# Kernel tuning notes

Measured on AMD Instinct MI355X. Metric: run time of the kernel, lower is better.

The kernel has to match this reference:

```python
import jax, jax.numpy as jnp
import numpy as np

N = 100000
E = 3200000
D_IN = 128
H = 32   # 2 * out_channels
OUT = 16 # out_channels


def _glorot(key, shape):
    lim = np.sqrt(6.0 / (shape[0] + shape[1]))
    return jax.random.uniform(key, shape, jnp.float32, -lim, lim)


def setup_inputs() -> dict:
    key = jax.random.key(0)
    ks = jax.random.split(key, 8)
    x = jax.random.normal(ks[0], (N, D_IN), jnp.float32)
    edge_index = jax.random.randint(ks[1], (2, E), 0, N, jnp.int64)
    W1 = _glorot(ks[2], (D_IN, H));  b1 = jnp.zeros((H,), jnp.float32)
    Wm = _glorot(ks[3], (H, OUT));   bm = jnp.zeros((OUT,), jnp.float32)
    Wv = _glorot(ks[4], (H, 1));     bv = jnp.zeros((1,), jnp.float32)
    return {"x": x, "edge_index": edge_index,
            "W1": W1, "b1": b1, "Wm": Wm, "bm": bm, "Wv": Wv, "bv": bv}


def _gcn_norm(edge_index, n_nodes):
    # add self-loops, then symmetric normalization D^-1/2 (A+I) D^-1/2
    loop = jnp.arange(n_nodes, dtype=edge_index.dtype)
    src = jnp.concatenate([edge_index[0], loop])
    dst = jnp.concatenate([edge_index[1], loop])
    deg = jax.ops.segment_sum(jnp.ones_like(dst, jnp.float32), dst,
                              num_segments=n_nodes)
    dinv = jnp.where(deg > 0, jax.lax.rsqrt(deg), 0.0)
    norm = dinv[src] * dinv[dst]  # [E + N]
    return src, dst, norm


def _gcn_conv(h, W, b, src, dst, norm, n_nodes):
    h = h @ W                                   # [N, out]
    msg = norm[:, None] * h[src]                # gather + scale, [E+N, out]
    out = jax.ops.segment_sum(msg, dst, num_segments=n_nodes)  # scatter-add
    return out + b


def reference(x, edge_index, W1, b1, Wm, bm, Wv, bv):
    src, dst, norm = _gcn_norm(edge_index, N)
    h = jax.nn.relu(_gcn_conv(x, W1, b1, src, dst, norm, N))
    mean = _gcn_conv(h, Wm, bm, src, dst, norm, N)
    mean = mean / jnp.linalg.norm(mean, axis=-1, keepdims=True)
    var = _gcn_conv(h, Wv, bv, src, dst, norm, N)
    var = jax.nn.softplus(var) + 1.0
    return mean, var
```

## Files before the change

### kernel.cpp

```cpp
#include <hip/hip_runtime.h>
#include <math.h>

#define N_NODES   100000
#define N_HALF    50000
#define N_EDGES   3200000
#define D_IN      128
#define H_DIM     32
#define OUT_DIM   16
#define NB        391
#define B1        1024
#define CHUNK     3125
#define NHIST     (NB * B1)
#define SUMS_N    (NHIST / 256)
#define SCANB_PER ((SUMS_N + 255) / 256)

typedef _Float16 half_t;
typedef __attribute__((ext_vector_type(4))) _Float16 half4;
typedef __attribute__((ext_vector_type(8))) _Float16 half8;


__global__ __launch_bounds__(256) void k_p1_hist(const int* __restrict__ dst,
                                                 int* __restrict__ hist_g) {
    __shared__ int hist[NB];
    int t = threadIdx.x;
    for (int i = t; i < NB; i += 256) hist[i] = 0;
    __syncthreads();
    int base = blockIdx.x * CHUNK;
    for (int k = t; k < CHUNK; k += 256)
        atomicAdd(&hist[dst[base + k] >> 8], 1);
    __syncthreads();
    for (int i = t; i < NB; i += 256) hist_g[i * B1 + blockIdx.x] = hist[i];
}


__global__ __launch_bounds__(256) void k_scanA(const int* __restrict__ hist_g,
                                               int* __restrict__ sums) {
    __shared__ int s[256];
    int t = threadIdx.x;
    s[t] = hist_g[blockIdx.x * 256 + t];
    __syncthreads();
    for (int off = 128; off > 0; off >>= 1) {
        if (t < off) s[t] += s[t + off];
        __syncthreads();
    }
    if (t == 0) sums[blockIdx.x] = s[0];
}

__global__ __launch_bounds__(256) void k_scanB(int* sums) {
    __shared__ int a[256], b[256];
    int t = threadIdx.x;
    int base = t * SCANB_PER;
    int v[SCANB_PER];
    int tot = 0;
#pragma unroll
    for (int k = 0; k < SCANB_PER; ++k) {
        v[k] = (base + k < SUMS_N) ? sums[base + k] : 0;
        tot += v[k];
    }
    a[t] = tot;
    __syncthreads();
    int* cur = a; int* nxt = b;
    for (int off = 1; off < 256; off <<= 1) {
        nxt[t] = cur[t] + ((t >= off) ? cur[t - off] : 0);
        __syncthreads();
        int* tmp = cur; cur = nxt; nxt = tmp;
    }
    int run = cur[t] - tot;
#pragma unroll
    for (int k = 0; k < SCANB_PER; ++k) {
        if (base + k < SUMS_N) sums[base + k] = run;
        run += v[k];
    }
}

__global__ __launch_bounds__(256) void k_scanC(int* hist_g, const int* __restrict__ sums) {
    __shared__ int a[256], b[256];
    int t = threadIdx.x;
    int v = hist_g[blockIdx.x * 256 + t];
    a[t] = v;
    __syncthreads();
    int* cur = a; int* nxt = b;
    for (int off = 1; off < 256; off <<= 1) {
        nxt[t] = cur[t] + ((t >= off) ? cur[t - off] : 0);
        __syncthreads();
        int* tmp = cur; cur = nxt; nxt = tmp;
    }
    hist_g[blockIdx.x * 256 + t] = sums[blockIdx.x] + cur[t] - v;
}


__global__ __launch_bounds__(256) void k_p3(const int* __restrict__ src,
                                            const int* __restrict__ dst,
                                            const int* __restrict__ hist_g,
                                            unsigned int* __restrict__ pairs) {
    __shared__ int cur[NB];
    int t = threadIdx.x;
    for (int i = t; i < NB; i += 256) cur[i] = hist_g[i * B1 + blockIdx.x];
    __syncthreads();
    int base = blockIdx.x * CHUNK;
    for (int k = t; k < CHUNK; k += 256) {
        int e = base + k;
        int d = dst[e];
        int pos = atomicAdd(&cur[d >> 8], 1);
        pairs[pos] = ((unsigned int)(d & 255) << 17) | (unsigned int)src[e];
    }
}


__global__ __launch_bounds__(512) void k_p4(const unsigned int* __restrict__ pairs,
                                            const int* __restrict__ hist_g,
                                            int* __restrict__ csr_src,
                                            int* __restrict__ row_ptr,
                                            int* __restrict__ row_mid,
                                            float* __restrict__ dinv) {
    __shared__ int cnt[512], a[512], b[512], cur[512];
    int t = threadIdx.x;
    int bk = blockIdx.x;
    int lo = hist_g[bk * B1];
    int hi = (bk + 1 < NB) ? hist_g[(bk + 1) * B1] : N_EDGES;

    cnt[t] = 0;
    __syncthreads();
    for (int j = lo + t; j < hi; j += 512) {
        unsigned int p = pairs[j];
        int s = (int)(p & 0x1FFFFu);
        int bin = (int)((p >> 17) << 1) | (s >= N_HALF);
        atomicAdd(&cnt[bin], 1);
    }
    __syncthreads();

    a[t] = cnt[t];
    __syncthreads();
    int* c0 = a; int* c1 = b;
    for (int off = 1; off < 512; off <<= 1) {
        c1[t] = c0[t] + ((t >= off) ? c0[t - off] : 0);
        __syncthreads();
        int* tmp = c0; c0 = c1; c1 = tmp;
    }
    int excl = c0[t] - cnt[t];
    cur[t] = lo + excl;

    int node = bk * 256 + (t >> 1);
    if (node < N_NODES) {
        if ((t & 1) == 0) {
            row_ptr[node] = lo + excl;
            dinv[node] = rsqrtf((float)(cnt[t] + cnt[t + 1]) + 1.0f);
        } else {
            row_mid[node] = lo + excl;
        }
    }
    if (bk == NB - 1 && t == 0) row_ptr[N_NODES] = N_EDGES;
    __syncthreads();

    for (int j = lo + t; j < hi; j += 512) {
        unsigned int p = pairs[j];
        int s = (int)(p & 0x1FFFFu);
        int bin = (int)((p >> 17) << 1) | (s >= N_HALF);
        int pos = atomicAdd(&cur[bin], 1);
        csr_src[pos] = s;
    }
}


__global__ __launch_bounds__(256) void k_gemm1(const float* __restrict__ x,
                                               const float* __restrict__ W1,
                                               const float* __restrict__ dinv,
                                               half_t* __restrict__ hs) {
    int i = blockIdx.x * 256 + threadIdx.x;
    if (i >= N_NODES) return;

    const float* xr = x + (size_t)i * D_IN;
    float acc[H_DIM];
#pragma unroll
    for (int c = 0; c < H_DIM; ++c) acc[c] = 0.f;

    for (int k0 = 0; k0 < D_IN; k0 += 4) {
        float4 xv = *(const float4*)(xr + k0);
#pragma unroll
        for (int kk = 0; kk < 4; ++kk) {
            float xk = (kk == 0) ? xv.x : (kk == 1) ? xv.y : (kk == 2) ? xv.z : xv.w;
            const float* wr = W1 + (k0 + kk) * H_DIM;
#pragma unroll
            for (int c = 0; c < H_DIM; ++c)
                acc[c] = fmaf(xk, wr[c], acc[c]);
        }
    }

    float di = dinv[i];
    half_t* o = hs + (size_t)i * H_DIM;
#pragma unroll
    for (int c4 = 0; c4 < H_DIM / 4; ++c4) {
        half4 ov;
        ov.x = (half_t)(acc[c4 * 4 + 0] * di);
        ov.y = (half_t)(acc[c4 * 4 + 1] * di);
        ov.z = (half_t)(acc[c4 * 4 + 2] * di);
        ov.w = (half_t)(acc[c4 * 4 + 3] * di);
        *(half4*)(o + c4 * 4) = ov;
    }
}


__global__ __launch_bounds__(256) void k_gather1A(const int* __restrict__ row_ptr,
                                                  const int* __restrict__ row_mid,
                                                  const int* __restrict__ csr_src,
                                                  const half_t* __restrict__ hs,
                                                  half_t* __restrict__ h_part) {
    int t = blockIdx.x * 256 + threadIdx.x;
    int i = t >> 2, c = t & 3;
    if (i >= N_NODES) return;

    const half8* hp = (const half8*)hs;
    int start = row_ptr[i], end = row_mid[i];
    float acc[8];
#pragma unroll
    for (int k = 0; k < 8; ++k) acc[k] = 0.f;

    int j = start;
    for (; j + 8 <= end; j += 8) {
        int s0 = csr_src[j + 0], s1 = csr_src[j + 1], s2 = csr_src[j + 2], s3 = csr_src[j + 3];
        int s4 = csr_src[j + 4], s5 = csr_src[j + 5], s6 = csr_src[j + 6], s7 = csr_src[j + 7];
        half8 v0 = hp[(size_t)s0 * 4 + c];
        half8 v1 = hp[(size_t)s1 * 4 + c];
        half8 v2 = hp[(size_t)s2 * 4 + c];
        half8 v3 = hp[(size_t)s3 * 4 + c];
        half8 v4 = hp[(size_t)s4 * 4 + c];
        half8 v5 = hp[(size_t)s5 * 4 + c];
        half8 v6 = hp[(size_t)s6 * 4 + c];
        half8 v7 = hp[(size_t)s7 * 4 + c];
#pragma unroll
        for (int k = 0; k < 8; ++k)
            acc[k] += ((float)v0[k] + (float)v1[k] + (float)v2[k] + (float)v3[k])
                    + ((float)v4[k] + (float)v5[k] + (float)v6[k] + (float)v7[k]);
    }
    for (; j < end; ++j) {
        int s = csr_src[j];
        half8 v = hp[(size_t)s * 4 + c];
#pragma unroll
        for (int k = 0; k < 8; ++k) acc[k] += (float)v[k];
    }

    half8 o;
#pragma unroll
    for (int k = 0; k < 8; ++k) o[k] = (half_t)acc[k];
    ((half8*)h_part)[(size_t)i * 4 + c] = o;
}


__global__ __launch_bounds__(256) void k_gather1B(const int* __restrict__ row_ptr,
                                                  const int* __restrict__ row_mid,
                                                  const int* __restrict__ csr_src,
                                                  const float* __restrict__ dinv,
                                                  const half_t* __restrict__ hs,
                                                  const half_t* __restrict__ h_part,
                                                  const float* __restrict__ b1,
                                                  half_t* __restrict__ h) {
    int t = blockIdx.x * 256 + threadIdx.x;
    int i = t >> 2, c = t & 3;
    if (i >= N_NODES) return;

    const half8* hp = (const half8*)hs;
    int start = row_mid[i], end = row_ptr[i + 1];
    half8 pv = ((const half8*)h_part)[(size_t)i * 4 + c];
    half8 sv = hp[(size_t)i * 4 + c];
    float acc[8];
#pragma unroll
    for (int k = 0; k < 8; ++k) acc[k] = (float)pv[k] + (float)sv[k];

    int j = start;
    for (; j + 8 <= end; j += 8) {
        int s0 = csr_src[j + 0], s1 = csr_src[j + 1], s2 = csr_src[j + 2], s3 = csr_src[j + 3];
        int s4 = csr_src[j + 4], s5 = csr_src[j + 5], s6 = csr_src[j + 6], s7 = csr_src[j + 7];
        half8 v0 = hp[(size_t)s0 * 4 + c];
        half8 v1 = hp[(size_t)s1 * 4 + c];
        half8 v2 = hp[(size_t)s2 * 4 + c];
        half8 v3 = hp[(size_t)s3 * 4 + c];
        half8 v4 = hp[(size_t)s4 * 4 + c];
        half8 v5 = hp[(size_t)s5 * 4 + c];
        half8 v6 = hp[(size_t)s6 * 4 + c];
        half8 v7 = hp[(size_t)s7 * 4 + c];
#pragma unroll
        for (int k = 0; k < 8; ++k)
            acc[k] += ((float)v0[k] + (float)v1[k] + (float)v2[k] + (float)v3[k])
                    + ((float)v4[k] + (float)v5[k] + (float)v6[k] + (float)v7[k]);
    }
    for (; j < end; ++j) {
        int s = csr_src[j];
        half8 v = hp[(size_t)s * 4 + c];
#pragma unroll
        for (int k = 0; k < 8; ++k) acc[k] += (float)v[k];
    }

    float di = dinv[i];
    float4 ba = *(const float4*)(b1 + c * 8);
    float4 bb = *(const float4*)(b1 + c * 8 + 4);
    half8 o;
    o[0] = (half_t)fmaxf(di * acc[0] + ba.x, 0.f);
    o[1] = (half_t)fmaxf(di * acc[1] + ba.y, 0.f);
    o[2] = (half_t)fmaxf(di * acc[2] + ba.z, 0.f);
    o[3] = (half_t)fmaxf(di * acc[3] + ba.w, 0.f);
    o[4] = (half_t)fmaxf(di * acc[4] + bb.x, 0.f);
    o[5] = (half_t)fmaxf(di * acc[5] + bb.y, 0.f);
    o[6] = (half_t)fmaxf(di * acc[6] + bb.z, 0.f);
    o[7] = (half_t)fmaxf(di * acc[7] + bb.w, 0.f);
    ((half8*)h)[(size_t)i * 4 + c] = o;
}


__global__ __launch_bounds__(256) void k_gemm2(const half_t* __restrict__ h,
                                               const float* __restrict__ Wm,
                                               const float* __restrict__ Wv,
                                               const float* __restrict__ dinv,
                                               half_t* __restrict__ hmv,
                                               float* __restrict__ varr) {
    int i = blockIdx.x * 256 + threadIdx.x;
    if (i >= N_NODES) return;

    const half4* hp = (const half4*)(h + (size_t)i * H_DIM);
    float acc[OUT_DIM + 1];
#pragma unroll
    for (int c = 0; c <= OUT_DIM; ++c) acc[c] = 0.f;

#pragma unroll
    for (int k4 = 0; k4 < H_DIM / 4; ++k4) {
        half4 v = hp[k4];
#pragma unroll
        for (int kk = 0; kk < 4; ++kk) {
            int k = k4 * 4 + kk;
            float hv = (kk == 0) ? (float)v.x : (kk == 1) ? (float)v.y
                     : (kk == 2) ? (float)v.z : (float)v.w;
            const float* wr = Wm + k * OUT_DIM;
#pragma unroll
            for (int c = 0; c < OUT_DIM; ++c)
                acc[c] = fmaf(hv, wr[c], acc[c]);
            acc[OUT_DIM] = fmaf(hv, Wv[k], acc[OUT_DIM]);
        }
    }

    float di = dinv[i];
    half_t* o = hmv + (size_t)i * OUT_DIM;
#pragma unroll
    for (int c4 = 0; c4 < OUT_DIM / 4; ++c4) {
        half4 ov;
        ov.x = (half_t)(acc[c4 * 4 + 0] * di);
        ov.y = (half_t)(acc[c4 * 4 + 1] * di);
        ov.z = (half_t)(acc[c4 * 4 + 2] * di);
        ov.w = (half_t)(acc[c4 * 4 + 3] * di);
        *(half4*)(o + c4 * 4) = ov;
    }
    varr[i] = acc[OUT_DIM] * di;
}


__global__ __launch_bounds__(256) void k_gather2f(const int* __restrict__ row_ptr,
                                                  const int* __restrict__ csr_src,
                                                  const float* __restrict__ dinv,
                                                  const half_t* __restrict__ hmv,
                                                  const float* __restrict__ varr,
                                                  const float* __restrict__ bm,
                                                  const float* __restrict__ bv,
                                                  float* __restrict__ out) {
    int t = blockIdx.x * 256 + threadIdx.x;
    int i = t >> 2, c = t & 3;
    if (i >= N_NODES) return;

    int start = row_ptr[i], end = row_ptr[i + 1];
    half4 sv = *(const half4*)(hmv + (size_t)i * OUT_DIM + c * 4);
    float a0 = (float)sv.x, a1 = (float)sv.y, a2 = (float)sv.z, a3 = (float)sv.w;
    float va = (c == 0) ? varr[i] : 0.f;

    int j = start;
    for (; j + 8 <= end; j += 8) {
        int s0 = csr_src[j + 0], s1 = csr_src[j + 1], s2 = csr_src[j + 2], s3 = csr_src[j + 3];
        int s4 = csr_src[j + 4], s5 = csr_src[j + 5], s6 = csr_src[j + 6], s7 = csr_src[j + 7];
        half4 v0 = *(const half4*)(hmv + (size_t)s0 * OUT_DIM + c * 4);
        half4 v1 = *(const half4*)(hmv + (size_t)s1 * OUT_DIM + c * 4);
        half4 v2 = *(const half4*)(hmv + (size_t)s2 * OUT_DIM + c * 4);
        half4 v3 = *(const half4*)(hmv + (size_t)s3 * OUT_DIM + c * 4);
        half4 v4 = *(const half4*)(hmv + (size_t)s4 * OUT_DIM + c * 4);
        half4 v5 = *(const half4*)(hmv + (size_t)s5 * OUT_DIM + c * 4);
        half4 v6 = *(const half4*)(hmv + (size_t)s6 * OUT_DIM + c * 4);
        half4 v7 = *(const half4*)(hmv + (size_t)s7 * OUT_DIM + c * 4);
        a0 += ((float)v0.x + (float)v1.x + (float)v2.x + (float)v3.x)
            + ((float)v4.x + (float)v5.x + (float)v6.x + (float)v7.x);
        a1 += ((float)v0.y + (float)v1.y + (float)v2.y + (float)v3.y)
            + ((float)v4.y + (float)v5.y + (float)v6.y + (float)v7.y);
        a2 += ((float)v0.z + (float)v1.z + (float)v2.z + (float)v3.z)
            + ((float)v4.z + (float)v5.z + (float)v6.z + (float)v7.z);
        a3 += ((float)v0.w + (float)v1.w + (float)v2.w + (float)v3.w)
            + ((float)v4.w + (float)v5.w + (float)v6.w + (float)v7.w);
        int sa = (c == 0) ? s0 : (c == 1) ? s1 : (c == 2) ? s2 : s3;
        int sb = (c == 0) ? s4 : (c == 1) ? s5 : (c == 2) ? s6 : s7;
        va += varr[sa] + varr[sb];
    }
    for (; j < end; ++j) {
        int s = csr_src[j];
        half4 v = *(const half4*)(hmv + (size_t)s * OUT_DIM + c * 4);
        a0 += (float)v.x; a1 += (float)v.y; a2 += (float)v.z; a3 += (float)v.w;
        if (c == 0) va += varr[s];
    }

    float di = dinv[i];
    float4 bb = *(const float4*)(bm + c * 4);
    float r0 = di * a0 + bb.x;
    float r1 = di * a1 + bb.y;
    float r2 = di * a2 + bb.z;
    float r3 = di * a3 + bb.w;
    float ssp = r0 * r0 + r1 * r1 + r2 * r2 + r3 * r3;
    ssp += __shfl_xor(ssp, 1, 4);
    ssp += __shfl_xor(ssp, 2, 4);
    va  += __shfl_xor(va, 1, 4);
    va  += __shfl_xor(va, 2, 4);
    float inv = rsqrtf(ssp);

    float4 o;
    o.x = r0 * inv; o.y = r1 * inv; o.z = r2 * inv; o.w = r3 * inv;
    *(float4*)(out + (size_t)i * OUT_DIM + c * 4) = o;
    if (c == 0) {
        float xv = di * va + bv[0];
        float sp = fmaxf(xv, 0.f) + log1pf(expf(-fabsf(xv)));
        out[(size_t)N_NODES * OUT_DIM + i] = sp + 1.0f;
    }
}


extern "C" void kernel_launch(void* const* d_in, const int* in_sizes, int n_in,
                              void* d_out, int out_size, void* d_ws, size_t ws_size,
                              hipStream_t stream) {
    const float* x  = (const float*)d_in[0];
    const int*   ei = (const int*)d_in[1];
    const float* W1 = (const float*)d_in[2];
    const float* b1 = (const float*)d_in[3];
    const float* Wm = (const float*)d_in[4];
    const float* bm = (const float*)d_in[5];
    const float* Wv = (const float*)d_in[6];
    const float* bv = (const float*)d_in[7];
    float* out = (float*)d_out;

    const int* src = ei;
    const int* dst = ei + N_EDGES;

    int*   wsi     = (int*)d_ws;
    int*   csr_src = wsi;
    int*   row_ptr = csr_src + N_EDGES;
    int*   row_mid = row_ptr + N_NODES + 1;
    float* dinv    = (float*)(row_mid + N_NODES);
    int*   hist_g  = (int*)(dinv + N_NODES);
    int*   sums    = hist_g + NHIST;
    size_t off     = (size_t)(sums + 2048 - wsi);
    off = (off + 3) & ~(size_t)3;
    unsigned int* pairs = (unsigned int*)(wsi + off);
    half_t* hs     = (half_t*)pairs;
    half_t* h      = hs + (size_t)N_NODES * H_DIM;
    half_t* hmv    = h + (size_t)N_NODES * H_DIM;
    float*  varr   = (float*)(hmv + (size_t)N_NODES * OUT_DIM);
    half_t* h_part = (half_t*)(varr + N_NODES);

    const int B = 256;
    int gN  = (N_NODES + B - 1) / B;
    int gN4 = (N_NODES * 4 + B - 1) / B;

    k_p1_hist<<<B1, B, 0, stream>>>(dst, hist_g);
    k_scanA<<<SUMS_N, B, 0, stream>>>(hist_g, sums);
    k_scanB<<<1, B, 0, stream>>>(sums);
    k_scanC<<<SUMS_N, B, 0, stream>>>(hist_g, sums);
    k_p3<<<B1, B, 0, stream>>>(src, dst, hist_g, pairs);
    k_p4<<<NB, 512, 0, stream>>>(pairs, hist_g, csr_src, row_ptr, row_mid, dinv);

    k_gemm1<<<gN, B, 0, stream>>>(x, W1, dinv, hs);
    k_gather1A<<<gN4, B, 0, stream>>>(row_ptr, row_mid, csr_src, hs, h_part);
    k_gather1B<<<gN4, B, 0, stream>>>(row_ptr, row_mid, csr_src, dinv, hs, h_part, b1, h);

    k_gemm2<<<gN, B, 0, stream>>>(h, Wm, Wv, dinv, hmv, varr);
    k_gather2f<<<gN4, B, 0, stream>>>(row_ptr, csr_src, dinv, hmv, varr, bm, bv, out);
}
```

Baseline: 311.1 us.

## Vectorize CSR build loads, halve sort blocks, widen gathers and gather2 lanes

Halves the number of histogram/scatter blocks (each now covers a larger chunk) and switches their edge reads to int4 vector loads with a scalar tail. The bucket-local sort in p4 is unrolled two-way. Layer-1 gathers now issue 16 independent row loads per step, and the final gather uses 2 lanes of 8 halves per node instead of 4 lanes of 4. The aim is fewer, wider memory transactions and more loads in flight, at the cost of lower block-level parallelism in the sort phases and higher register pressure.

```diff
diff --git a/kernel.cpp b/kernel.cpp
--- a/kernel.cpp
+++ b/kernel.cpp
@@ -8,15 +8,17 @@
 #define H_DIM     32
 #define OUT_DIM   16
 #define NB        391
-#define B1        1024
-#define CHUNK     3125
+#define B1        512
+#define CHUNK     6272
 #define NHIST     (NB * B1)
 #define SUMS_N    (NHIST / 256)
-#define SCANB_PER ((SUMS_N + 255) / 256)
+#define SCANB_PER 4
 
 typedef _Float16 half_t;
 typedef __attribute__((ext_vector_type(4))) _Float16 half4;
 typedef __attribute__((ext_vector_type(8))) _Float16 half8;
+
+#define PACK(d, s) ((((unsigned int)(d) & 255u) << 17) | (unsigned int)(s))
 
 
 __global__ __launch_bounds__(256) void k_p1_hist(const int* __restrict__ dst,
@@ -26,8 +28,19 @@
     for (int i = t; i < NB; i += 256) hist[i] = 0;
     __syncthreads();
     int base = blockIdx.x * CHUNK;
-    for (int k = t; k < CHUNK; k += 256)
-        atomicAdd(&hist[dst[base + k] >> 8], 1);
+    for (int k = t * 4; k < CHUNK; k += 1024) {
+        int e = base + k;
+        if (k + 4 <= CHUNK && e + 4 <= N_EDGES) {
+            int4 d = *(const int4*)(dst + e);
+            atomicAdd(&hist[d.x >> 8], 1);
+            atomicAdd(&hist[d.y >> 8], 1);
+            atomicAdd(&hist[d.z >> 8], 1);
+            atomicAdd(&hist[d.w >> 8], 1);
+        } else {
+            for (int kk = k; kk < CHUNK && base + kk < N_EDGES; ++kk)
+                atomicAdd(&hist[dst[base + kk] >> 8], 1);
+        }
+    }
     __syncthreads();
     for (int i = t; i < NB; i += 256) hist_g[i * B1 + blockIdx.x] = hist[i];
 }
@@ -98,11 +111,26 @@
     for (int i = t; i < NB; i += 256) cur[i] = hist_g[i * B1 + blockIdx.x];
     __syncthreads();
     int base = blockIdx.x * CHUNK;
-    for (int k = t; k < CHUNK; k += 256) {
+    for (int k = t * 4; k < CHUNK; k += 1024) {
         int e = base + k;
-        int d = dst[e];
-        int pos = atomicAdd(&cur[d >> 8], 1);
-        pairs[pos] = ((unsigned int)(d & 255) << 17) | (unsigned int)src[e];
+        if (k + 4 <= CHUNK && e + 4 <= N_EDGES) {
+            int4 d = *(const int4*)(dst + e);
+            int4 s = *(const int4*)(src + e);
+            int p0 = atomicAdd(&cur[d.x >> 8], 1);
+            int p1 = atomicAdd(&cur[d.y >> 8], 1);
+            int p2 = atomicAdd(&cur[d.z >> 8], 1);
+            int p3 = atomicAdd(&cur[d.w >> 8], 1);
+            pairs[p0] = PACK(d.x, s.x);
+            pairs[p1] = PACK(d.y, s.y);
+            pairs[p2] = PACK(d.z, s.z);
+            pairs[p3] = PACK(d.w, s.w);
+        } else {
+            for (int kk = k; kk < CHUNK && base + kk < N_EDGES; ++kk) {
+                int d = dst[base + kk];
+                int pos = atomicAdd(&cur[d >> 8], 1);
+                pairs[pos] = PACK(d, src[base + kk]);
+            }
+        }
     }
 }
 
@@ -121,11 +149,19 @@
 
     cnt[t] = 0;
     __syncthreads();
-    for (int j = lo + t; j < hi; j += 512) {
-        unsigned int p = pairs[j];
-        int s = (int)(p & 0x1FFFFu);
-        int bin = (int)((p >> 17) << 1) | (s >= N_HALF);
-        atomicAdd(&cnt[bin], 1);
+    {
+        int j = lo + t;
+        for (; j + 512 < hi; j += 1024) {
+            unsigned int p = pairs[j], q = pairs[j + 512];
+            int sp = (int)(p & 0x1FFFFu), sq = (int)(q & 0x1FFFFu);
+            atomicAdd(&cnt[(int)((p >> 17) << 1) | (sp >= N_HALF)], 1);
+            atomicAdd(&cnt[(int)((q >> 17) << 1) | (sq >= N_HALF)], 1);
+        }
+        for (; j < hi; j += 512) {
+            unsigned int p = pairs[j];
+            int sp = (int)(p & 0x1FFFFu);
+            atomicAdd(&cnt[(int)((p >> 17) << 1) | (sp >= N_HALF)], 1);
+        }
     }
     __syncthreads();
 
@@ -152,12 +188,22 @@
     if (bk == NB - 1 && t == 0) row_ptr[N_NODES] = N_EDGES;
     __syncthreads();
 
-    for (int j = lo + t; j < hi; j += 512) {
-        unsigned int p = pairs[j];
-        int s = (int)(p & 0x1FFFFu);
-        int bin = (int)((p >> 17) << 1) | (s >= N_HALF);
-        int pos = atomicAdd(&cur[bin], 1);
-        csr_src[pos] = s;
+    {
+        int j = lo + t;
+        for (; j + 512 < hi; j += 1024) {
+            unsigned int p = pairs[j], q = pairs[j + 512];
+            int sp = (int)(p & 0x1FFFFu), sq = (int)(q & 0x1FFFFu);
+            int pp = atomicAdd(&cur[(int)((p >> 17) << 1) | (sp >= N_HALF)], 1);
+            int pq = atomicAdd(&cur[(int)((q >> 17) << 1) | (sq >= N_HALF)], 1);
+            csr_src[pp] = sp;
+            csr_src[pq] = sq;
+        }
+        for (; j < hi; j += 512) {
+            unsigned int p = pairs[j];
+            int sp = (int)(p & 0x1FFFFu);
+            int pp = atomicAdd(&cur[(int)((p >> 17) << 1) | (sp >= N_HALF)], 1);
+            csr_src[pp] = sp;
+        }
     }
 }
 
@@ -197,6 +243,37 @@
         ov.w = (half_t)(acc[c4 * 4 + 3] * di);
         *(half4*)(o + c4 * 4) = ov;
     }
+}
+
+
+__device__ __forceinline__ void acc16(const half8* __restrict__ hp,
+                                      const int* __restrict__ csr, int j, int c,
+                                      float acc[8]) {
+    int s[16];
+#pragma unroll
+    for (int u = 0; u < 16; ++u) s[u] = csr[j + u];
+    half8 v[16];
+#pragma unroll
+    for (int u = 0; u < 16; ++u) v[u] = hp[(size_t)s[u] * 4 + c];
+#pragma unroll
+    for (int u = 0; u < 16; ++u)
+#pragma unroll
+        for (int k = 0; k < 8; ++k) acc[k] += (float)v[u][k];
+}
+
+__device__ __forceinline__ void acc4(const half8* __restrict__ hp,
+                                     const int* __restrict__ csr, int j, int c,
+                                     float acc[8]) {
+    int s[4];
+#pragma unroll
+    for (int u = 0; u < 4; ++u) s[u] = csr[j + u];
+    half8 v[4];
+#pragma unroll
+    for (int u = 0; u < 4; ++u) v[u] = hp[(size_t)s[u] * 4 + c];
+#pragma unroll
+    for (int u = 0; u < 4; ++u)
+#pragma unroll
+        for (int k = 0; k < 8; ++k) acc[k] += (float)v[u][k];
 }
 
 
@@ -216,25 +293,10 @@
     for (int k = 0; k < 8; ++k) acc[k] = 0.f;
 
     int j = start;
-    for (; j + 8 <= end; j += 8) {
-        int s0 = csr_src[j + 0], s1 = csr_src[j + 1], s2 = csr_src[j + 2], s3 = csr_src[j + 3];
-        int s4 = csr_src[j + 4], s5 = csr_src[j + 5], s6 = csr_src[j + 6], s7 = csr_src[j + 7];
-        half8 v0 = hp[(size_t)s0 * 4 + c];
-        half8 v1 = hp[(size_t)s1 * 4 + c];
-        half8 v2 = hp[(size_t)s2 * 4 + c];
-        half8 v3 = hp[(size_t)s3 * 4 + c];
-        half8 v4 = hp[(size_t)s4 * 4 + c];
-        half8 v5 = hp[(size_t)s5 * 4 + c];
-        half8 v6 = hp[(size_t)s6 * 4 + c];
-        half8 v7 = hp[(size_t)s7 * 4 + c];
-#pragma unroll
-        for (int k = 0; k < 8; ++k)
-            acc[k] += ((float)v0[k] + (float)v1[k] + (float)v2[k] + (float)v3[k])
-                    + ((float)v4[k] + (float)v5[k] + (float)v6[k] + (float)v7[k]);
-    }
+    for (; j + 16 <= end; j += 16) acc16(hp, csr_src, j, c, acc);
+    for (; j + 4 <= end; j += 4)  acc4(hp, csr_src, j, c, acc);
     for (; j < end; ++j) {
-        int s = csr_src[j];
-        half8 v = hp[(size_t)s * 4 + c];
+        half8 v = hp[(size_t)csr_src[j] * 4 + c];
 #pragma unroll
         for (int k = 0; k < 8; ++k) acc[k] += (float)v[k];
     }
@@ -267,25 +329,10 @@
     for (int k = 0; k < 8; ++k) acc[k] = (float)pv[k] + (float)sv[k];
 
     int j = start;
-    for (; j + 8 <= end; j += 8) {
-        int s0 = csr_src[j + 0], s1 = csr_src[j + 1], s2 = csr_src[j + 2], s3 = csr_src[j + 3];
-        int s4 = csr_src[j + 4], s5 = csr_src[j + 5], s6 = csr_src[j + 6], s7 = csr_src[j + 7];
-        half8 v0 = hp[(size_t)s0 * 4 + c];
-        half8 v1 = hp[(size_t)s1 * 4 + c];
-        half8 v2 = hp[(size_t)s2 * 4 + c];
-        half8 v3 = hp[(size_t)s3 * 4 + c];
-        half8 v4 = hp[(size_t)s4 * 4 + c];
-        half8 v5 = hp[(size_t)s5 * 4 + c];
-        half8 v6 = hp[(size_t)s6 * 4 + c];
-        half8 v7 = hp[(size_t)s7 * 4 + c];
-#pragma unroll
-        for (int k = 0; k < 8; ++k)
-            acc[k] += ((float)v0[k] + (float)v1[k] + (float)v2[k] + (float)v3[k])
-                    + ((float)v4[k] + (float)v5[k] + (float)v6[k] + (float)v7[k]);
-    }
+    for (; j + 16 <= end; j += 16) acc16(hp, csr_src, j, c, acc);
+    for (; j + 4 <= end; j += 4)  acc4(hp, csr_src, j, c, acc);
     for (; j < end; ++j) {
-        int s = csr_src[j];
-        half8 v = hp[(size_t)s * 4 + c];
+        half8 v = hp[(size_t)csr_src[j] * 4 + c];
 #pragma unroll
         for (int k = 0; k < 8; ++k) acc[k] += (float)v[k];
     }
@@ -360,61 +407,62 @@
                                                   const float* __restrict__ bv,
                                                   float* __restrict__ out) {
     int t = blockIdx.x * 256 + threadIdx.x;
-    int i = t >> 2, c = t & 3;
+    int i = t >> 1, c = t & 1;
     if (i >= N_NODES) return;
 
+    const half8* mp = (const half8*)hmv;
     int start = row_ptr[i], end = row_ptr[i + 1];
-    half4 sv = *(const half4*)(hmv + (size_t)i * OUT_DIM + c * 4);
-    float a0 = (float)sv.x, a1 = (float)sv.y, a2 = (float)sv.z, a3 = (float)sv.w;
+    half8 sv = mp[(size_t)i * 2 + c];
+    float acc[8];
+#pragma unroll
+    for (int k = 0; k < 8; ++k) acc[k] = (float)sv[k];
     float va = (c == 0) ? varr[i] : 0.f;
 
     int j = start;
     for (; j + 8 <= end; j += 8) {
-        int s0 = csr_src[j + 0], s1 = csr_src[j + 1], s2 = csr_src[j + 2], s3 = csr_src[j + 3];
-        int s4 = csr_src[j + 4], s5 = csr_src[j + 5], s6 = csr_src[j + 6], s7 = csr_src[j + 7];
-        half4 v0 = *(const half4*)(hmv + (size_t)s0 * OUT_DIM + c * 4);
-        half4 v1 = *(const half4*)(hmv + (size_t)s1 * OUT_DIM + c * 4);
-        half4 v2 = *(const half4*)(hmv + (size_t)s2 * OUT_DIM + c * 4);
-        half4 v3 = *(const half4*)(hmv + (size_t)s3 * OUT_DIM + c * 4);
-        half4 v4 = *(const half4*)(hmv + (size_t)s4 * OUT_DIM + c * 4);
-        half4 v5 = *(const half4*)(hmv + (size_t)s5 * OUT_DIM + c * 4);
-        half4 v6 = *(const half4*)(hmv + (size_t)s6 * OUT_DIM + c * 4);
-        half4 v7 = *(const half4*)(hmv + (size_t)s7 * OUT_DIM + c * 4);
-        a0 += ((float)v0.x + (float)v1.x + (float)v2.x + (float)v3.x)
-            + ((float)v4.x + (float)v5.x + (float)v6.x + (float)v7.x);
-        a1 += ((float)v0.y + (float)v1.y + (float)v2.y + (float)v3.y)
-            + ((float)v4.y + (float)v5.y + (float)v6.y + (float)v7.y);
-        a2 += ((float)v0.z + (float)v1.z + (float)v2.z + (float)v3.z)
-            + ((float)v4.z + (float)v5.z + (float)v6.z + (float)v7.z);
-        a3 += ((float)v0.w + (float)v1.w + (float)v2.w + (float)v3.w)
-            + ((float)v4.w + (float)v5.w + (float)v6.w + (float)v7.w);
-        int sa = (c == 0) ? s0 : (c == 1) ? s1 : (c == 2) ? s2 : s3;
-        int sb = (c == 0) ? s4 : (c == 1) ? s5 : (c == 2) ? s6 : s7;
-        va += varr[sa] + varr[sb];
+        int s[8];
+#pragma unroll
+        for (int u = 0; u < 8; ++u) s[u] = csr_src[j + u];
+        half8 v[8];
+#pragma unroll
+        for (int u = 0; u < 8; ++u) v[u] = mp[(size_t)s[u] * 2 + c];
+        float va0 = varr[s[c]], va1 = varr[s[c + 2]];
+        float va2 = varr[s[c + 4]], va3 = varr[s[c + 6]];
+#pragma unroll
+        for (int u = 0; u < 8; ++u)
+#pragma unroll
+            for (int k = 0; k < 8; ++k) acc[k] += (float)v[u][k];
+        va += (va0 + va1) + (va2 + va3);
     }
     for (; j < end; ++j) {
         int s = csr_src[j];
-        half4 v = *(const half4*)(hmv + (size_t)s * OUT_DIM + c * 4);
-        a0 += (float)v.x; a1 += (float)v.y; a2 += (float)v.z; a3 += (float)v.w;
+        half8 v = mp[(size_t)s * 2 + c];
+#pragma unroll
+        for (int k = 0; k < 8; ++k) acc[k] += (float)v[k];
         if (c == 0) va += varr[s];
     }
 
     float di = dinv[i];
-    float4 bb = *(const float4*)(bm + c * 4);
-    float r0 = di * a0 + bb.x;
-    float r1 = di * a1 + bb.y;
-    float r2 = di * a2 + bb.z;
-    float r3 = di * a3 + bb.w;
-    float ssp = r0 * r0 + r1 * r1 + r2 * r2 + r3 * r3;
-    ssp += __shfl_xor(ssp, 1, 4);
-    ssp += __shfl_xor(ssp, 2, 4);
-    va  += __shfl_xor(va, 1, 4);
-    va  += __shfl_xor(va, 2, 4);
+    float4 ba = *(const float4*)(bm + c * 8);
+    float4 bb = *(const float4*)(bm + c * 8 + 4);
+    float r[8];
+    r[0] = di * acc[0] + ba.x;  r[1] = di * acc[1] + ba.y;
+    r[2] = di * acc[2] + ba.z;  r[3] = di * acc[3] + ba.w;
+    r[4] = di * acc[4] + bb.x;  r[5] = di * acc[5] + bb.y;
+    r[6] = di * acc[6] + bb.z;  r[7] = di * acc[7] + bb.w;
+    float ssp = 0.f;
+#pragma unroll
+    for (int k = 0; k < 8; ++k) ssp += r[k] * r[k];
+    ssp += __shfl_xor(ssp, 1, 2);
+    va  += __shfl_xor(va, 1, 2);
     float inv = rsqrtf(ssp);
 
-    float4 o;
-    o.x = r0 * inv; o.y = r1 * inv; o.z = r2 * inv; o.w = r3 * inv;
-    *(float4*)(out + (size_t)i * OUT_DIM + c * 4) = o;
+    float* op = out + (size_t)i * OUT_DIM + c * 8;
+    float4 o0, o1;
+    o0.x = r[0] * inv; o0.y = r[1] * inv; o0.z = r[2] * inv; o0.w = r[3] * inv;
+    o1.x = r[4] * inv; o1.y = r[5] * inv; o1.z = r[6] * inv; o1.w = r[7] * inv;
+    *(float4*)op = o0;
+    *(float4*)(op + 4) = o1;
     if (c == 0) {
         float xv = di * va + bv[0];
         float sp = fmaxf(xv, 0.f) + log1pf(expf(-fabsf(xv)));
@@ -446,7 +494,7 @@
     float* dinv    = (float*)(row_mid + N_NODES);
     int*   hist_g  = (int*)(dinv + N_NODES);
     int*   sums    = hist_g + NHIST;
-    size_t off     = (size_t)(sums + 2048 - wsi);
+    size_t off     = (size_t)(sums + 1024 - wsi);
     off = (off + 3) & ~(size_t)3;
     unsigned int* pairs = (unsigned int*)(wsi + off);
     half_t* hs     = (half_t*)pairs;
@@ -458,6 +506,7 @@
     const int B = 256;
     int gN  = (N_NODES + B - 1) / B;
     int gN4 = (N_NODES * 4 + B - 1) / B;
+    int gN2 = (N_NODES * 2 + B - 1) / B;
 
     k_p1_hist<<<B1, B, 0, stream>>>(dst, hist_g);
     k_scanA<<<SUMS_N, B, 0, stream>>>(hist_g, sums);
@@ -471,5 +520,5 @@
     k_gather1B<<<gN4, B, 0, stream>>>(row_ptr, row_mid, csr_src, dinv, hs, h_part, b1, h);
 
     k_gemm2<<<gN, B, 0, stream>>>(h, Wm, Wv, dinv, hmv, varr);
-    k_gather2f<<<gN4, B, 0, stream>>>(row_ptr, csr_src, dinv, hmv, varr, bm, bv, out);
-}
+    k_gather2f<<<gN2, B, 0, stream>>>(row_ptr, csr_src, dinv, hmv, varr, bm, bv, out);
+}
```

Result: faster. 297.1 us (-4.5%).
